# Kernel tuning notes

Hardware: AMD Instinct MI355X
Metric: run time of the kernel (lower is better)

Reference implementation:

```python
import jax, jax.numpy as jnp
import numpy as np

N = 200000   # total atoms in batched graph
E = 3200000  # total bonds (directed edges)
B = 512      # number of graphs / sequences
L = 1000     # miRNA sequence length


def _gcn(x, W, b, src, dst, dis):
    # PyG GCNConv: add self-loops, symmetric normalization D^-1/2 A D^-1/2
    h = x @ W                                   # [N, Fout]
    msg = (dis[src] * dis[dst])[:, None] * h[src]
    agg = jax.ops.segment_sum(msg, dst, num_segments=x.shape[0])
    return agg + (dis * dis)[:, None] * h + b   # self-loop term + bias


def _conv1d(x, k, b):
    # x: [B, C, L], k: [O, I, K]  (torch Conv1d, VALID padding)
    y = jax.lax.conv_general_dilated(x, k, (1,), 'VALID',
                                     dimension_numbers=('NCH', 'OIH', 'NCH'))
    return y + b[None, :, None]


def _mp3(x):
    # torch MaxPool1d(3): window 3, stride 3, floor
    return jax.lax.reduce_window(x, -jnp.inf, jax.lax.max, (1, 1, 3), (1, 1, 3), 'VALID')


def setup_inputs() -> dict:
    key = jax.random.key(0)
    ks = jax.random.split(key, 24)
    w = lambda k, s: (jax.random.normal(k, s, jnp.float32) * 0.1)
    p = {}
    p['x'] = jax.random.normal(ks[0], (N, 4), jnp.float32)
    p['edge_index'] = jax.random.randint(ks[1], (2, E), 0, N, jnp.int32)
    p['batch'] = (jnp.arange(N, dtype=jnp.int32) * B // N).astype(jnp.int32)  # every graph non-empty
    p['target'] = jax.random.normal(ks[2], (B, L, 5), jnp.float32)
    # GCN layers 4->4->8->16
    p['W1'] = w(ks[3], (4, 4));    p['b1'] = jnp.zeros(4, jnp.float32)
    p['W2'] = w(ks[4], (4, 8));    p['b2'] = jnp.zeros(8, jnp.float32)
    p['W3'] = w(ks[5], (8, 16));   p['b3'] = jnp.zeros(16, jnp.float32)
    p['Wg1'] = w(ks[6], (16, 1024)); p['bg1'] = jnp.zeros(1024, jnp.float32)
    p['Wg2'] = w(ks[7], (1024, 128)); p['bg2'] = jnp.zeros(128, jnp.float32)
    # CNN stack on sequences, kernels [O, I, 8]
    p['K1'] = w(ks[8], (32, 5, 8));   p['cb1'] = jnp.zeros(32, jnp.float32)
    p['K2'] = w(ks[9], (64, 32, 8));  p['cb2'] = jnp.zeros(64, jnp.float32)
    p['K3'] = w(ks[10], (128, 64, 8)); p['cb3'] = jnp.zeros(128, jnp.float32)
    p['Wxt'] = w(ks[11], (128, 128)); p['bxt'] = jnp.zeros(128, jnp.float32)
    # fusion head
    p['Wf1'] = w(ks[12], (256, 1024)); p['bf1'] = jnp.zeros(1024, jnp.float32)
    p['Wf2'] = w(ks[13], (1024, 512)); p['bf2'] = jnp.zeros(512, jnp.float32)
    p['Wo'] = w(ks[14], (512, 2));     p['bo'] = jnp.zeros(2, jnp.float32)
    return p


def reference(x, edge_index, batch, target, W1, b1, W2, b2, W3, b3,
              Wg1, bg1, Wg2, bg2, K1, cb1, K2, cb2, K3, cb3,
              Wxt, bxt, Wf1, bf1, Wf2, bf2, Wo, bo):
    src, dst = edge_index[0], edge_index[1]
    deg = jax.ops.segment_sum(jnp.ones(src.shape[0], x.dtype), dst,
                              num_segments=x.shape[0]) + 1.0  # +1 self-loop
    dis = jax.lax.rsqrt(deg)
    # Graph branch (dropout is identity in eval)
    h = jax.nn.relu(_gcn(x, W1, b1, src, dst, dis))
    h = jax.nn.relu(_gcn(h, W2, b2, src, dst, dis))
    h = jax.nn.relu(_gcn(h, W3, b3, src, dst, dis))
    g = jax.ops.segment_max(h, batch, num_segments=B)  # global_max_pool
    g = jax.nn.relu(g @ Wg1 + bg1)
    g = g @ Wg2 + bg2
    # Sequence branch
    t = jnp.transpose(target, (0, 2, 1))  # [B, 5, L]
    c = _mp3(jax.nn.relu(_conv1d(t, K1, cb1)))
    c = _mp3(jax.nn.relu(_conv1d(c, K2, cb2)))
    c = _mp3(jax.nn.relu(_conv1d(c, K3, cb3)))
    c = jnp.mean(c, axis=2)               # [B, 128]
    c = jax.nn.relu(c @ Wxt + bxt)
    # Fusion head
    xc = jnp.concatenate([g, c], axis=1)  # [B, 256]
    xc = jax.nn.relu(xc @ Wf1 + bf1)
    xc = jax.nn.relu(xc @ Wf2 + bf2)
    return xc @ Wo + bo                    # [B, 2]
```

## Files before the change

kernel.cpp:

```cpp
#include <hip/hip_runtime.h>
#include <hip/hip_fp16.h>
#include <cstddef>

#define NA 200000
#define NE 3200000
#define NB 512
#define NBKT 256
#define BKTN 782
#define BKTCAP 16384
#define NEPB 3200
#define NGB 3125

typedef _Float16 hv2 __attribute__((ext_vector_type(2)));
typedef _Float16 half8 __attribute__((ext_vector_type(8)));
typedef float floatx4 __attribute__((ext_vector_type(4)));
union UH2 { unsigned u; __half2 h; hv2 v; };
__device__ __forceinline__ float4 h4f(unsigned a, unsigned b) {
    UH2 x, y; x.u = a; y.u = b;
    float2 fa = __half22float2(x.h), fb = __half22float2(y.h);
    return make_float4(fa.x, fa.y, fb.x, fb.y);
}
__device__ __forceinline__ unsigned f2h(float a, float b) {
    UH2 r; r.h = __float22half2_rn(make_float2(a, b));
    return r.u;
}

__global__ void k_init(unsigned* g, int* gcursor,
                       float* gvec, const float* __restrict__ bg2,
                       float* xf2, const float* __restrict__ bf2,
                       float* xf1, const float* __restrict__ bf1,
                       const float* __restrict__ K2, const float* __restrict__ K3,
                       __half* __restrict__ Wt2, __half* __restrict__ Wt3) {
    int i = blockIdx.x * blockDim.x + threadIdx.x;
    if (i < NB * 16) g[i] = 0u;
    if (i < NBKT) gcursor[i] = i * BKTCAP;
    if (i < NB * 128) gvec[i] = bg2[i & 127];
    if (i < NB * 512) xf2[i] = bf2[i & 511];
    if (i < NB * 1024) xf1[i] = bf1[i & 1023];
    if (i < 64 * 32 * 8) {
        int o = i >> 8, rem = i & 255, c = rem >> 3, kk = rem & 7;
        Wt2[(o << 8) + (kk << 5) + c] = __float2half(K2[i]);
    }
    if (i < 128 * 64 * 8) {
        int o = i >> 9, rem = i & 511, c = rem >> 3, kk = rem & 7;
        Wt3[(o << 9) + (kk << 6) + c] = __float2half(K3[i]);
    }
}

template<int CIN, int COUT, int OBLK, int LIN, int PITCH, int POUT, int NTT>
__device__ __forceinline__ void dev_conv1(int b, int oy,
        const float* __restrict__ in, const float* __restrict__ Kw,
        const float* __restrict__ bias, __half* __restrict__ out,
        float* s_in) {
    constexpr int SPO = 256 / OBLK;
    constexpr int PT = (NTT < 4) ? NTT : 4;
    constexpr int NPASS = (NTT + PT - 1) / PT;
    for (int idx = threadIdx.x; idx < CIN * PITCH; idx += 256) s_in[idx] = 0.f;
    __syncthreads();
    for (int idx = threadIdx.x; idx < LIN * CIN; idx += 256) {
        int p = idx / CIN, c = idx - p * CIN;
        s_in[c * PITCH + p] = in[(size_t)b * (LIN * CIN) + idx];
    }
    __syncthreads();
    int ol = threadIdx.x / SPO;
    int s  = threadIdx.x - ol * SPO;
    int o  = oy * OBLK + ol;
    float bo = bias[o];
    const float* wrow = Kw + (size_t)o * CIN * 8;
    for (int pass = 0; pass < NPASS; pass++) {
        float acc[PT][12];
#pragma unroll
        for (int tt = 0; tt < PT; tt++)
#pragma unroll
            for (int j = 0; j < 12; j++) acc[tt][j] = 0.f;
        bool vld[PT]; int tgs[PT];
#pragma unroll
        for (int tt = 0; tt < PT; tt++) {
            int ta = pass * PT + tt;
            int tg = s + SPO * ta;
            tgs[tt] = tg;
            vld[tt] = (ta < NTT) && (4 * tg < POUT);
        }
        for (int i = 0; i < CIN; i++) {
            float wa[8];
            const float4* wp = (const float4*)(wrow + (size_t)i * 8);
            *(float4*)&wa[0] = wp[0];
            *(float4*)&wa[4] = wp[1];
#pragma unroll
            for (int tt = 0; tt < PT; tt++) {
                if (vld[tt]) {
                    const float4* xr = (const float4*)&s_in[i * PITCH + 12 * tgs[tt]];
                    float xa[20];
#pragma unroll
                    for (int q = 0; q < 5; q++) *(float4*)&xa[4 * q] = xr[q];
#pragma unroll
                    for (int j = 0; j < 12; j++) {
                        float sm = acc[tt][j];
#pragma unroll
                        for (int k = 0; k < 8; k++) sm = fmaf(xa[j + k], wa[k], sm);
                        acc[tt][j] = sm;
                    }
                }
            }
        }
#pragma unroll
        for (int tt = 0; tt < PT; tt++) {
            if (vld[tt]) {
#pragma unroll
                for (int p = 0; p < 4; p++) {
                    int P = 4 * tgs[tt] + p;
                    if (P < POUT) {
                        float m = fmaxf(fmaxf(acc[tt][3 * p], acc[tt][3 * p + 1]), acc[tt][3 * p + 2]);
                        out[((size_t)b * COUT + o) * POUT + P] = __float2half(fmaxf(m + bo, 0.f));
                    }
                }
            }
        }
    }
}

__device__ __forceinline__ void dev_conv2_mfma(int b,
        const __half* __restrict__ pool1, const __half* __restrict__ Wt2,
        const float* __restrict__ cb2, __half* __restrict__ pool2t,
        char* smem) {
    __half* sT   = (__half*)smem;
    __half* outS = (__half*)smem;
    const __half* inp = pool1 + (size_t)b * (32 * 331);
    for (int idx = threadIdx.x; idx < 32 * 331; idx += 256) {
        int c = idx / 331;
        int p = idx - c * 331;
        sT[p * 40 + c] = inp[idx];
    }
    __syncthreads();
    int lane = threadIdx.x & 63, wv = threadIdx.x >> 6;
    int l15 = lane & 15, lg = lane >> 4;
    int mtBeg = wv * 5;
    int nmt = (wv == 3) ? 6 : 5;
    const floatx4 FZ = {0.f, 0.f, 0.f, 0.f};
    floatx4 acc[6][4];
#pragma unroll
    for (int mi = 0; mi < 6; mi++)
#pragma unroll
        for (int nt = 0; nt < 4; nt++) acc[mi][nt] = FZ;
    const half8* WB = (const half8*)Wt2;
    for (int s = 0; s < 8; s++) {
        half8 bfr[4];
#pragma unroll
        for (int nt = 0; nt < 4; nt++)
            bfr[nt] = WB[(nt * 16 + l15) * 32 + s * 4 + lg];
        half8 afr[6];
#pragma unroll
        for (int mi = 0; mi < 6; mi++) {
            if (mi < nmt) {
                int row = (mtBeg + mi) * 16 + l15 + s;
                afr[mi] = *(const half8*)(sT + row * 40 + lg * 8);
            }
        }
#pragma unroll
        for (int mi = 0; mi < 6; mi++) {
            if (mi < nmt) {
#pragma unroll
                for (int nt = 0; nt < 4; nt++)
                    acc[mi][nt] = __builtin_amdgcn_mfma_f32_16x16x32_f16(
                        afr[mi], bfr[nt], acc[mi][nt], 0, 0, 0);
            }
        }
    }
    __syncthreads();
    float bo[4];
#pragma unroll
    for (int nt = 0; nt < 4; nt++) bo[nt] = cb2[nt * 16 + l15];
#pragma unroll
    for (int mi = 0; mi < 6; mi++) {
        if (mi < nmt) {
#pragma unroll
            for (int nt = 0; nt < 4; nt++) {
                int o = nt * 16 + l15;
#pragma unroll
                for (int r = 0; r < 4; r++) {
                    int p = (mtBeg + mi) * 16 + lg * 4 + r;
                    float v = fmaxf(acc[mi][nt][r] + bo[nt], 0.f);
                    outS[p * 68 + o] = __float2half(v);
                }
            }
        }
    }
    __syncthreads();
    __half* op = pool2t + (size_t)b * (108 * 64);
    for (int idx = threadIdx.x; idx < 108 * 64; idx += 256) {
        int P = idx >> 6, o = idx & 63;
        float v0 = __half2float(outS[(3 * P) * 68 + o]);
        float v1 = __half2float(outS[(3 * P + 1) * 68 + o]);
        float v2 = __half2float(outS[(3 * P + 2) * 68 + o]);
        op[idx] = __float2half(fmaxf(fmaxf(v0, v1), v2));
    }
}

__device__ __forceinline__ void dev_conv3_mfma(int b, int nh,
        const __half* __restrict__ pool2t, const __half* __restrict__ Wt3,
        const float* __restrict__ cb3, float* __restrict__ pool3,
        char* smem) {
    __half* sT  = (__half*)smem;
    float* outS = (float*)smem;
    const uint4* inp = (const uint4*)(pool2t + (size_t)b * (108 * 64));
    for (int t = threadIdx.x; t < 108 * 8; t += 256) {
        int r = t >> 3, s8 = t & 7;
        *(uint4*)(sT + r * 72 + s8 * 8) = inp[t];
    }
    __syncthreads();
    int lane = threadIdx.x & 63, wv = threadIdx.x >> 6;
    int l15 = lane & 15, lg = lane >> 4;
    int mtBeg = wv * 2;
    int nmt = (wv == 3) ? 1 : 2;
    const floatx4 FZ = {0.f, 0.f, 0.f, 0.f};
    floatx4 acc[2][4];
#pragma unroll
    for (int mi = 0; mi < 2; mi++)
#pragma unroll
        for (int nt = 0; nt < 4; nt++) acc[mi][nt] = FZ;
    const half8* WB = (const half8*)Wt3;
    for (int s = 0; s < 16; s++) {
        half8 afr[2];
#pragma unroll
        for (int mi = 0; mi < 2; mi++) {
            if (mi < nmt) {
                int row = (mtBeg + mi) * 16 + l15 + (s >> 1);
                afr[mi] = *(const half8*)(sT + row * 72 + (s & 1) * 32 + lg * 8);
            }
        }
#pragma unroll
        for (int nt = 0; nt < 4; nt++) {
            half8 bfr = WB[((nh * 4 + nt) * 16 + l15) * 64 + s * 4 + lg];
            acc[0][nt] = __builtin_amdgcn_mfma_f32_16x16x32_f16(
                afr[0], bfr, acc[0][nt], 0, 0, 0);
            if (nmt > 1)
                acc[1][nt] = __builtin_amdgcn_mfma_f32_16x16x32_f16(
                    afr[1], bfr, acc[1][nt], 0, 0, 0);
        }
    }
    __syncthreads();
    float bo[4];
#pragma unroll
    for (int nt = 0; nt < 4; nt++) bo[nt] = cb3[(nh * 4 + nt) * 16 + l15];
    float* op = pool3 + (size_t)b * (33 * 128);
    for (int pp = 0; pp < 3; pp++) {
        int t0 = 3 * pp;
#pragma unroll
        for (int mi = 0; mi < 2; mi++) {
            int tile = mtBeg + mi;
            if (mi < nmt && tile >= t0 && tile < t0 + 3) {
#pragma unroll
                for (int nt = 0; nt < 4; nt++) {
                    int ol = nt * 16 + l15;
#pragma unroll
                    for (int r = 0; r < 4; r++) {
                        int p = tile * 16 + lg * 4 + r;
                        if (p < 100)
                            outS[(p - 48 * pp) * 68 + ol] =
                                fmaxf(acc[mi][nt][r] + bo[nt], 0.f);
                    }
                }
            }
        }
        __syncthreads();
        int nP = (pp == 2) ? 1 : 16;
        for (int idx = threadIdx.x; idx < nP * 64; idx += 256) {
            int Pl = idx >> 6, ol = idx & 63;
            int P = 16 * pp + Pl;
            int p = 3 * P - 48 * pp;
            float v0 = outS[p * 68 + ol];
            float v1 = outS[(p + 1) * 68 + ol];
            float v2 = outS[(p + 2) * 68 + ol];
            op[P * 128 + (nh << 6) + ol] = fmaxf(fmaxf(v0, v1), v2);
        }
        __syncthreads();
    }
}

__global__ __launch_bounds__(256) void k_A(
        const int* __restrict__ src, const int* __restrict__ dst,
        int* __restrict__ gcursor, unsigned* __restrict__ stage,
        const float* __restrict__ tgt, const float* __restrict__ K1,
        const float* __restrict__ cb1, __half* __restrict__ pool1) {
    __shared__ __align__(16) char smem[20160];
    int bx = blockIdx.x;
    if (bx < 1024) {
        dev_conv1<5, 32, 16, 1000, 1008, 331, 6>(bx >> 1, bx & 1, tgt, K1, cb1,
                                                 pool1, (float*)smem);
        return;
    }
    int* hcnt  = (int*)smem;
    int* hbase = hcnt + 256;
    int* lbase = hbase + 256;
    unsigned* sbuf = (unsigned*)(lbase + 256);
    unsigned char* sbkt = (unsigned char*)(sbuf + NEPB);
    int t = threadIdx.x;
    int e0 = (bx - 1024) * NEPB;
    hcnt[t] = 0;
    __syncthreads();
    const int4* d4 = (const int4*)(dst + e0);
    for (int i = t; i < NEPB / 4; i += 256) {
        int4 d = d4[i];
        atomicAdd(&hcnt[d.x / BKTN], 1);
        atomicAdd(&hcnt[d.y / BKTN], 1);
        atomicAdd(&hcnt[d.z / BKTN], 1);
        atomicAdd(&hcnt[d.w / BKTN], 1);
    }
    __syncthreads();
    int myc = hcnt[t];
    hbase[t] = atomicAdd(&gcursor[t], myc);
    __syncthreads();
#pragma unroll
    for (int off = 1; off < 256; off <<= 1) {
        int u = (t >= off) ? hcnt[t - off] : 0;
        __syncthreads();
        hcnt[t] += u;
        __syncthreads();
    }
    lbase[t] = hcnt[t] - myc;
    hcnt[t] = 0;
    __syncthreads();
    const int4* s4 = (const int4*)(src + e0);
    for (int i = t; i < NEPB / 4; i += 256) {
        int4 d = d4[i];
        int4 s = s4[i];
        int ds[4] = {d.x, d.y, d.z, d.w};
        int ss[4] = {s.x, s.y, s.z, s.w};
#pragma unroll
        for (int j = 0; j < 4; j++) {
            int bkt = ds[j] / BKTN;
            int dloc = ds[j] - bkt * BKTN;
            int k = atomicAdd(&hcnt[bkt], 1);
            int pos = lbase[bkt] + k;
            sbuf[pos] = ((unsigned)dloc << 18) | (unsigned)ss[j];
            sbkt[pos] = (unsigned char)bkt;
        }
    }
    __syncthreads();
    for (int i = t; i < NEPB; i += 256) {
        unsigned v = sbuf[i];
        int bkt = sbkt[i];
        stage[hbase[bkt] + (i - lbase[bkt])] = v;
    }
}

__global__ __launch_bounds__(256) void k_Bp(
        const unsigned* __restrict__ stage, const int* __restrict__ gcursor,
        int* __restrict__ rowptr, int* __restrict__ cnt, int* __restrict__ csr,
        const float* __restrict__ x, float4* __restrict__ dt1) {
    __shared__ int lcnt[BKTN];
    __shared__ int lpos[BKTN];
    __shared__ int partial[256];
    __shared__ int sbase;
    int t = threadIdx.x;
    int bkt = blockIdx.x;
    int tot = gcursor[t] - t * BKTCAP;
    partial[t] = tot;
    __syncthreads();
#pragma unroll
    for (int off = 1; off < 256; off <<= 1) {
        int u = (t >= off) ? partial[t - off] : 0;
        __syncthreads();
        partial[t] += u;
        __syncthreads();
    }
    if (t == 0) sbase = (bkt == 0) ? 0 : partial[bkt - 1];
    __syncthreads();
    int base = sbase;
    int n0 = bkt * BKTN;
    int ncnt = (NA - n0 < BKTN) ? (NA - n0) : BKTN;
    int eBeg = bkt * BKTCAP;
    int eCnt = gcursor[bkt] - eBeg;
    for (int i = t; i < BKTN; i += 256) lcnt[i] = 0;
    __syncthreads();
    for (int i = t; i < eCnt; i += 256)
        atomicAdd(&lcnt[stage[eBeg + i] >> 18], 1);
    __syncthreads();
    int mysum = 0;
#pragma unroll
    for (int j = 0; j < 4; j++) {
        int node = 4 * t + j;
        if (node < ncnt) mysum += lcnt[node];
    }
    partial[t] = mysum;
    __syncthreads();
#pragma unroll
    for (int off = 1; off < 256; off <<= 1) {
        int u = (t >= off) ? partial[t - off] : 0;
        __syncthreads();
        partial[t] += u;
        __syncthreads();
    }
    int running = partial[t] - mysum;
#pragma unroll
    for (int j = 0; j < 4; j++) {
        int node = 4 * t + j;
        if (node < ncnt) {
            lpos[node] = running;
            rowptr[n0 + node] = base + running;
            cnt[n0 + node] = lcnt[node];
            running += lcnt[node];
        }
    }
    __syncthreads();
    for (int i = t; i < eCnt; i += 256) {
        unsigned v = stage[eBeg + i];
        int dloc = v >> 18;
        int s = v & 0x3FFFF;
        int k = atomicAdd(&lpos[dloc], 1);
        csr[base + k] = s;
    }
    for (int i = t; i < ncnt; i += 256) {
        int n = n0 + i;
        float4 p = ((const float4*)x)[n];
        float dv = rsqrtf((float)lcnt[i] + 1.0f);
        dt1[n] = make_float4(dv * p.x, dv * p.y, dv * p.z, dv * p.w);
    }
}

__global__ __launch_bounds__(256) void k_B(
        const __half* __restrict__ pool1, const __half* __restrict__ Wt2,
        const float* __restrict__ cb2, __half* __restrict__ pool2t,
        const float4* __restrict__ dt1, const int* __restrict__ rowptr,
        const int* __restrict__ cnt, const int* __restrict__ csr,
        const float* __restrict__ W1, const float* __restrict__ b1,
        float* __restrict__ dt2f) {
    __shared__ __align__(16) char smem[45696];
    int bx = blockIdx.x;
    if (bx < 512) {
        dev_conv2_mfma(bx, pool1, Wt2, cb2, pool2t, smem);
        return;
    }
    __shared__ float sW[16];
    if (threadIdx.x < 16) sW[threadIdx.x] = W1[threadIdx.x];
    __syncthreads();
    int n   = (bx - 512) * 64 + (threadIdx.x >> 2);
    int sub = threadIdx.x & 3;
    int cn = cnt[n];
    float dv = rsqrtf((float)cn + 1.0f);
    const int* row = csr + rowptr[n];
    float4 selfv = dt1[n];
    float4 acc = make_float4(0.f, 0.f, 0.f, 0.f);
    if (sub == 0) acc = selfv;
    int e = sub;
    for (; e + 12 < cn; e += 16) {
        float4 v0 = dt1[row[e]];
        float4 v1 = dt1[row[e + 4]];
        float4 v2 = dt1[row[e + 8]];
        float4 v3 = dt1[row[e + 12]];
        acc.x += (v0.x + v1.x) + (v2.x + v3.x);
        acc.y += (v0.y + v1.y) + (v2.y + v3.y);
        acc.z += (v0.z + v1.z) + (v2.z + v3.z);
        acc.w += (v0.w + v1.w) + (v2.w + v3.w);
    }
    for (; e < cn; e += 4) {
        float4 v = dt1[row[e]];
        acc.x += v.x; acc.y += v.y; acc.z += v.z; acc.w += v.w;
    }
    acc.x += __shfl_xor(acc.x, 1); acc.y += __shfl_xor(acc.y, 1);
    acc.z += __shfl_xor(acc.z, 1); acc.w += __shfl_xor(acc.w, 1);
    acc.x += __shfl_xor(acc.x, 2); acc.y += __shfl_xor(acc.y, 2);
    acc.z += __shfl_xor(acc.z, 2); acc.w += __shfl_xor(acc.w, 2);
    float a[4] = {acc.x, acc.y, acc.z, acc.w};
    float s = 0.f;
#pragma unroll
    for (int k = 0; k < 4; k++) s = fmaf(a[k], sW[k * 4 + sub], s);
    float o = dv * fmaxf(fmaf(dv, s, b1[sub]), 0.f);
    dt2f[(size_t)n * 4 + sub] = o;
}

__global__ __launch_bounds__(256, 8) void k_C(
        const __half* __restrict__ pool2t, const __half* __restrict__ Wt3,
        const float* __restrict__ cb3, float* __restrict__ pool3,
        const float4* __restrict__ dt2, const int* __restrict__ rowptr,
        const int* __restrict__ cnt, const int* __restrict__ csr,
        const float* __restrict__ W2, const float* __restrict__ b2,
        unsigned* __restrict__ dt3u) {
    __shared__ __align__(16) char smem[17280];
    int bx = blockIdx.x;
    if (bx < 1024) {
        dev_conv3_mfma(bx & 511, bx >> 9, pool2t, Wt3, cb3, pool3, smem);
        return;
    }
    __shared__ float sW[32];
    if (threadIdx.x < 32) sW[threadIdx.x] = W2[threadIdx.x];
    __syncthreads();
    int n   = (bx - 1024) * 64 + (threadIdx.x >> 2);
    int sub = threadIdx.x & 3;
    int cn = cnt[n];
    float dv = rsqrtf((float)cn + 1.0f);
    const int* row = csr + rowptr[n];
    float4 selfv = dt2[n];
    float4 acc = make_float4(0.f, 0.f, 0.f, 0.f);
    if (sub == 0) acc = selfv;
    int e = sub;
    for (; e + 12 < cn; e += 16) {
        float4 v0 = dt2[row[e]];
        float4 v1 = dt2[row[e + 4]];
        float4 v2 = dt2[row[e + 8]];
        float4 v3 = dt2[row[e + 12]];
        acc.x += (v0.x + v1.x) + (v2.x + v3.x);
        acc.y += (v0.y + v1.y) + (v2.y + v3.y);
        acc.z += (v0.z + v1.z) + (v2.z + v3.z);
        acc.w += (v0.w + v1.w) + (v2.w + v3.w);
    }
    for (; e < cn; e += 4) {
        float4 v = dt2[row[e]];
        acc.x += v.x; acc.y += v.y; acc.z += v.z; acc.w += v.w;
    }
    acc.x += __shfl_xor(acc.x, 1); acc.y += __shfl_xor(acc.y, 1);
    acc.z += __shfl_xor(acc.z, 1); acc.w += __shfl_xor(acc.w, 1);
    acc.x += __shfl_xor(acc.x, 2); acc.y += __shfl_xor(acc.y, 2);
    acc.z += __shfl_xor(acc.z, 2); acc.w += __shfl_xor(acc.w, 2);
    float a[4] = {acc.x, acc.y, acc.z, acc.w};
    int f0 = 2 * sub;
    float s0 = 0.f, s1 = 0.f;
#pragma unroll
    for (int k = 0; k < 4; k++) {
        s0 = fmaf(a[k], sW[k * 8 + f0], s0);
        s1 = fmaf(a[k], sW[k * 8 + f0 + 1], s1);
    }
    float o0 = dv * fmaxf(fmaf(dv, s0, b2[f0]), 0.f);
    float o1 = dv * fmaxf(fmaf(dv, s1, b2[f0 + 1]), 0.f);
    dt3u[(size_t)n * 4 + sub] = f2h(o0, o1);
}

__global__ __launch_bounds__(256) void k_D(
        const uint4* __restrict__ dt3, const int* __restrict__ rowptr,
        const int* __restrict__ cnt, const int* __restrict__ csr,
        const float* __restrict__ W3, const float* __restrict__ b3,
        const int* __restrict__ batch, unsigned* __restrict__ g,
        const float* __restrict__ pool3, const float* __restrict__ Wxt,
        const float* __restrict__ bxt, float* __restrict__ cx) {
    int bx = blockIdx.x;
    if (bx >= NGB) {
        __shared__ float sa[8 * 128];
        int b0 = (bx - NGB) * 8;
        for (int t = threadIdx.x; t < 8 * 128; t += 256) {
            int gg = t >> 7, k = t & 127;
            const float* r = pool3 + (size_t)(b0 + gg) * (33 * 128) + k;
            float s = 0.f;
#pragma unroll
            for (int p = 0; p < 33; p++) s += r[p * 128];
            sa[t] = s * (1.f / 33.f);
        }
        __syncthreads();
        int j = threadIdx.x;
        if (j >= 128) return;
        float bj = bxt[j];
        float acc[8];
#pragma unroll
        for (int gg = 0; gg < 8; gg++) acc[gg] = bj;
#pragma unroll 4
        for (int k = 0; k < 128; k++) {
            float w = Wxt[(size_t)k * 128 + j];
#pragma unroll
            for (int gg = 0; gg < 8; gg++) acc[gg] = fmaf(sa[gg * 128 + k], w, acc[gg]);
        }
#pragma unroll
        for (int gg = 0; gg < 8; gg++)
            cx[(size_t)(b0 + gg) * 128 + j] = fmaxf(acc[gg], 0.f);
        return;
    }
    __shared__ float sW[128];
    __shared__ unsigned sg[32];
    __shared__ int sbmin;
    if (threadIdx.x < 128) sW[threadIdx.x] = W3[threadIdx.x];
    if (threadIdx.x < 32) sg[threadIdx.x] = 0u;
    if (threadIdx.x == 0) sbmin = batch[bx * 64];
    __syncthreads();
    int n   = bx * 64 + (threadIdx.x >> 2);
    int sub = threadIdx.x & 3;
    int cn = cnt[n];
    float dv = rsqrtf((float)cn + 1.0f);
    const int* row = csr + rowptr[n];
    uint4 sv = dt3[n];
    float4 slo = h4f(sv.x, sv.y), shi = h4f(sv.z, sv.w);
    float a0 = 0.f, a1 = 0.f, a2 = 0.f, a3 = 0.f;
    float a4 = 0.f, a5 = 0.f, a6 = 0.f, a7 = 0.f;
    if (sub == 0) {
        a0 = slo.x; a1 = slo.y; a2 = slo.z; a3 = slo.w;
        a4 = shi.x; a5 = shi.y; a6 = shi.z; a7 = shi.w;
    }
    int e = sub;
    for (; e + 12 < cn; e += 16) {
        uint4 p0 = dt3[row[e]], p1 = dt3[row[e + 4]];
        uint4 p2 = dt3[row[e + 8]], p3 = dt3[row[e + 12]];
        float4 l0 = h4f(p0.x, p0.y), h0 = h4f(p0.z, p0.w);
        float4 l1 = h4f(p1.x, p1.y), h1 = h4f(p1.z, p1.w);
        float4 l2 = h4f(p2.x, p2.y), h2 = h4f(p2.z, p2.w);
        float4 l3 = h4f(p3.x, p3.y), h3v = h4f(p3.z, p3.w);
        a0 += (l0.x + l1.x) + (l2.x + l3.x);
        a1 += (l0.y + l1.y) + (l2.y + l3.y);
        a2 += (l0.z + l1.z) + (l2.z + l3.z);
        a3 += (l0.w + l1.w) + (l2.w + l3.w);
        a4 += (h0.x + h1.x) + (h2.x + h3v.x);
        a5 += (h0.y + h1.y) + (h2.y + h3v.y);
        a6 += (h0.z + h1.z) + (h2.z + h3v.z);
        a7 += (h0.w + h1.w) + (h2.w + h3v.w);
    }
    for (; e < cn; e += 4) {
        uint4 p = dt3[row[e]];
        float4 l = h4f(p.x, p.y), h = h4f(p.z, p.w);
        a0 += l.x; a1 += l.y; a2 += l.z; a3 += l.w;
        a4 += h.x; a5 += h.y; a6 += h.z; a7 += h.w;
    }
    a0 += __shfl_xor(a0, 1); a1 += __shfl_xor(a1, 1);
    a2 += __shfl_xor(a2, 1); a3 += __shfl_xor(a3, 1);
    a4 += __shfl_xor(a4, 1); a5 += __shfl_xor(a5, 1);
    a6 += __shfl_xor(a6, 1); a7 += __shfl_xor(a7, 1);
    a0 += __shfl_xor(a0, 2); a1 += __shfl_xor(a1, 2);
    a2 += __shfl_xor(a2, 2); a3 += __shfl_xor(a3, 2);
    a4 += __shfl_xor(a4, 2); a5 += __shfl_xor(a5, 2);
    a6 += __shfl_xor(a6, 2); a7 += __shfl_xor(a7, 2);
    float af[8] = {a0, a1, a2, a3, a4, a5, a6, a7};
    int rb = batch[n] - sbmin;
    if (rb > 1) rb = 1;
#pragma unroll
    for (int j = 0; j < 4; j++) {
        int f = sub * 4 + j;
        float s = 0.f;
#pragma unroll
        for (int k = 0; k < 8; k++) s = fmaf(af[k], sW[k * 16 + f], s);
        float r = fmaxf(fmaf(dv, s, b3[f]), 0.f);
        atomicMax(&sg[rb * 16 + f], __float_as_uint(r));
    }
    __syncthreads();
    if (threadIdx.x < 32) {
        unsigned v = sg[threadIdx.x];
        int rb2 = threadIdx.x >> 4, f = threadIdx.x & 15;
        int bbn = sbmin + rb2;
        if (v != 0u && bbn < NB) atomicMax(&g[bbn * 16 + f], v);
    }
}

__global__ __launch_bounds__(256) void k_head_g(
        const float* __restrict__ g, const float* __restrict__ Wg1,
        const float* __restrict__ bg1, float* __restrict__ gp1) {
    __shared__ float sa[8 * 16];
    int bx = blockIdx.x;
    int b0 = (bx >> 2) * 8;
    if (threadIdx.x < 128)
        sa[threadIdx.x] = g[b0 * 16 + threadIdx.x];
    __syncthreads();
    int j = (bx & 3) * 256 + threadIdx.x;
    float bj = bg1[j];
    float acc[8];
#pragma unroll
    for (int gg = 0; gg < 8; gg++) acc[gg] = bj;
#pragma unroll
    for (int k = 0; k < 16; k++) {
        float w = Wg1[(size_t)k * 1024 + j];
#pragma unroll
        for (int gg = 0; gg < 8; gg++) acc[gg] = fmaf(sa[gg * 16 + k], w, acc[gg]);
    }
#pragma unroll
    for (int gg = 0; gg < 8; gg++)
        gp1[(size_t)(b0 + gg) * 1024 + j] = fmaxf(acc[gg], 0.f);
}

__global__ __launch_bounds__(256) void k_gvec_ks(
        const float* __restrict__ gp1, const float* __restrict__ Wg2,
        float* __restrict__ gvec) {
    __shared__ float sa[8 * 128];
    int k0 = blockIdx.x * 128;
    int b0 = blockIdx.y * 8;
    for (int t = threadIdx.x; t < 8 * 128; t += 256) {
        int gg = t >> 7, k = t & 127;
        sa[t] = gp1[(size_t)(b0 + gg) * 1024 + k0 + k];
    }
    __syncthreads();
    int j  = threadIdx.x & 127;
    int kh = (threadIdx.x >> 7) * 64;
    const float* Wp = Wg2 + (size_t)(k0 + kh) * 128 + j;
    float acc[8];
#pragma unroll
    for (int gg = 0; gg < 8; gg++) acc[gg] = 0.f;
    for (int k = 0; k < 64; k += 16) {
        float w[16];
#pragma unroll
        for (int u = 0; u < 16; u++) w[u] = Wp[(size_t)(k + u) * 128];
#pragma unroll
        for (int u = 0; u < 16; u++) {
#pragma unroll
            for (int gg = 0; gg < 8; gg++)
                acc[gg] = fmaf(sa[gg * 128 + kh + k + u], w[u], acc[gg]);
        }
    }
#pragma unroll
    for (int gg = 0; gg < 8; gg++)
        atomicAdd(&gvec[(size_t)(b0 + gg) * 128 + j], acc[gg]);
}

__global__ __launch_bounds__(256) void k_cat2(
        const float* __restrict__ gvec, const float* __restrict__ cx,
        const float* __restrict__ Wf1, float* __restrict__ xf1) {
    __shared__ float sa[8 * 128];
    int jx = blockIdx.x & 3;
    int kh = blockIdx.x >> 2;
    int b0 = blockIdx.y * 8;
    const float* A = kh ? cx : gvec;
    for (int t = threadIdx.x; t < 8 * 128; t += 256) {
        int gg = t >> 7, k = t & 127;
        sa[t] = A[(size_t)(b0 + gg) * 128 + k];
    }
    __syncthreads();
    int j = jx * 256 + threadIdx.x;
    const float* Wp = Wf1 + (size_t)(kh * 128) * 1024 + j;
    float acc[8];
#pragma unroll
    for (int gg = 0; gg < 8; gg++) acc[gg] = 0.f;
    for (int k = 0; k < 128; k += 16) {
        float w[16];
#pragma unroll
        for (int u = 0; u < 16; u++) w[u] = Wp[(size_t)(k + u) * 1024];
#pragma unroll
        for (int u = 0; u < 16; u++) {
#pragma unroll
            for (int gg = 0; gg < 8; gg++)
                acc[gg] = fmaf(sa[gg * 128 + k + u], w[u], acc[gg]);
        }
    }
#pragma unroll
    for (int gg = 0; gg < 8; gg++)
        atomicAdd(&xf1[(size_t)(b0 + gg) * 1024 + j], acc[gg]);
}

__global__ __launch_bounds__(256) void k_xf2_ks(
        const float* __restrict__ xf1, const float* __restrict__ Wf2,
        float* __restrict__ xf2) {
    __shared__ float sa[8 * 256];
    int jb = blockIdx.x & 1;
    int k0 = (blockIdx.x >> 1) * 256;
    int b0 = blockIdx.y * 8;
    for (int t = threadIdx.x; t < 8 * 256; t += 256) {
        int gg = t >> 8, k = t & 255;
        sa[t] = fmaxf(xf1[(size_t)(b0 + gg) * 1024 + k0 + k], 0.f);
    }
    __syncthreads();
    int j = jb * 256 + threadIdx.x;
    const float* Wp = Wf2 + (size_t)k0 * 512 + j;
    float acc[8];
#pragma unroll
    for (int gg = 0; gg < 8; gg++) acc[gg] = 0.f;
    for (int k = 0; k < 256; k += 16) {
        float w[16];
#pragma unroll
        for (int u = 0; u < 16; u++) w[u] = Wp[(size_t)(k + u) * 512];
#pragma unroll
        for (int u = 0; u < 16; u++) {
#pragma unroll
            for (int gg = 0; gg < 8; gg++)
                acc[gg] = fmaf(sa[gg * 256 + k + u], w[u], acc[gg]);
        }
    }
#pragma unroll
    for (int gg = 0; gg < 8; gg++)
        atomicAdd(&xf2[(size_t)(b0 + gg) * 512 + j], acc[gg]);
}

__global__ __launch_bounds__(256) void k_dense_out(
        const float* __restrict__ A, const float* __restrict__ W,
        const float* __restrict__ bias, float* __restrict__ out) {
    int idx = blockIdx.x * 256 + threadIdx.x;
    if (idx >= NB * 2) return;
    int b = idx >> 1, j = idx & 1;
    float s = bias[j];
    const float4* A4 = (const float4*)(A + (size_t)b * 512);
    for (int k4 = 0; k4 < 128; k4 += 8) {
        float4 av[8];
#pragma unroll
        for (int u = 0; u < 8; u++) av[u] = A4[k4 + u];
#pragma unroll
        for (int u = 0; u < 8; u++) {
            int kb = (k4 + u) * 4;
            s = fmaf(fmaxf(av[u].x, 0.f), W[(kb + 0) * 2 + j], s);
            s = fmaf(fmaxf(av[u].y, 0.f), W[(kb + 1) * 2 + j], s);
            s = fmaf(fmaxf(av[u].z, 0.f), W[(kb + 2) * 2 + j], s);
            s = fmaf(fmaxf(av[u].w, 0.f), W[(kb + 3) * 2 + j], s);
        }
    }
    out[idx] = s;
}

extern "C" void kernel_launch(void* const* d_in, const int* in_sizes, int n_in,
                              void* d_out, int out_size, void* d_ws, size_t ws_size,
                              hipStream_t stream) {
    (void)in_sizes; (void)n_in; (void)out_size; (void)ws_size;
    const float* x   = (const float*)d_in[0];
    const int*  ei   = (const int*)d_in[1];
    const int*  batch= (const int*)d_in[2];
    const float* tgt = (const float*)d_in[3];
    const float* W1  = (const float*)d_in[4];  const float* b1  = (const float*)d_in[5];
    const float* W2  = (const float*)d_in[6];  const float* b2  = (const float*)d_in[7];
    const float* W3  = (const float*)d_in[8];  const float* b3  = (const float*)d_in[9];
    const float* Wg1 = (const float*)d_in[10]; const float* bg1 = (const float*)d_in[11];
    const float* Wg2 = (const float*)d_in[12]; const float* bg2 = (const float*)d_in[13];
    const float* K1  = (const float*)d_in[14]; const float* cb1 = (const float*)d_in[15];
    const float* K2  = (const float*)d_in[16]; const float* cb2 = (const float*)d_in[17];
    const float* K3  = (const float*)d_in[18]; const float* cb3 = (const float*)d_in[19];
    const float* Wxt = (const float*)d_in[20]; const float* bxt = (const float*)d_in[21];
    const float* Wf1 = (const float*)d_in[22]; const float* bf1 = (const float*)d_in[23];
    const float* Wf2 = (const float*)d_in[24]; const float* bf2 = (const float*)d_in[25];
    const float* Wo  = (const float*)d_in[26]; const float* bo  = (const float*)d_in[27];
    const int* srcp = ei;
    const int* dstp = ei + NE;

    float* ws = (float*)d_ws;
    float4* dt1 = (float4*)ws; ws += (size_t)NA * 4;
    float4* dt2 = (float4*)ws; ws += (size_t)NA * 4;
    uint4*  dt3 = (uint4*)ws;  ws += (size_t)NA * 4;
    float* g     = ws; ws += NB * 16;
    float* gp1   = ws; ws += NB * 1024;
    float* gvec  = ws; ws += NB * 128;
    float* cx    = ws; ws += NB * 128;
    float* xf1   = ws; ws += NB * 1024;
    float* xf2   = ws; ws += NB * 512;
    __half* pool1 = (__half*)ws; ws += (size_t)NB * 32 * 331;
    __half* pool2t = (__half*)ws; ws += (size_t)NB * 64 * 108;
    float* pool3 = ws; ws += (size_t)NB * 128 * 33;
    __half* Wt2 = (__half*)ws; ws += 64 * 256 / 2;
    __half* Wt3 = (__half*)ws; ws += 128 * 512 / 2;
    int*   cnt    = (int*)ws; ws += NA;
    int*   rowptr = (int*)ws; ws += NA;
    int*   csr    = (int*)ws; ws += NE;
    int*   gcursor= (int*)ws; ws += NBKT;
    unsigned* stage = (unsigned*)ws; ws += (size_t)NBKT * BKTCAP;

    dim3 blk(256);

    k_init<<<2048, blk, 0, stream>>>((unsigned*)g, gcursor, gvec, bg2, xf2, bf2,
                                     xf1, bf1, K2, K3, Wt2, Wt3);
    k_A<<<2024, blk, 0, stream>>>(srcp, dstp, gcursor, stage, tgt, K1, cb1, pool1);
    k_Bp<<<256, blk, 0, stream>>>(stage, gcursor, rowptr, cnt, csr, x, dt1);
    k_B<<<512 + NGB, blk, 0, stream>>>(pool1, Wt2, cb2, pool2t,
                                       dt1, rowptr, cnt, csr, W1, b1, (float*)dt2);
    k_C<<<1024 + NGB, blk, 0, stream>>>(pool2t, Wt3, cb3, pool3,
                                        dt2, rowptr, cnt, csr, W2, b2, (unsigned*)dt3);
    k_D<<<NGB + 64, blk, 0, stream>>>(dt3, rowptr, cnt, csr, W3, b3,
                                      batch, (unsigned*)g, pool3, Wxt, bxt, cx);

    k_head_g<<<256, blk, 0, stream>>>(g, Wg1, bg1, gp1);
    k_gvec_ks<<<dim3(8, 64), blk, 0, stream>>>(gp1, Wg2, gvec);
    k_cat2<<<dim3(8, 64), blk, 0, stream>>>(gvec, cx, Wf1, xf1);
    k_xf2_ks<<<dim3(8, 64), blk, 0, stream>>>(xf1, Wf2, xf2);
    k_dense_out<<<4, blk, 0, stream>>>(xf2, Wo, bo, (float*)d_out);
}
```

Baseline: 393.9 us.

## Move first conv1d layer onto MFMA f16 matrix cores with im2col-style fragments

Replaces the scalar FP32 direct convolution for the first Conv1d (5->32 channels, kernel 8) with an MFMA 16x16x32 f16 implementation. Input channels are padded to 8 and the weights are pre-packed into an fp16 buffer in the init kernel. Each block now covers a third of a sequence instead of half the output channels, and the conv blocks are placed after the edge-bucketing blocks in the fused launch. The change trades FP32 precision for fp16 inputs and adds extra shared-memory staging for the pooling step.

After: 402.0 us. +2.1%, slower.

```diff
diff --git a/kernel.cpp b/kernel.cpp
--- a/kernel.cpp
+++ b/kernel.cpp
@@ -29,14 +29,21 @@
                        float* gvec, const float* __restrict__ bg2,
                        float* xf2, const float* __restrict__ bf2,
                        float* xf1, const float* __restrict__ bf1,
-                       const float* __restrict__ K2, const float* __restrict__ K3,
-                       __half* __restrict__ Wt2, __half* __restrict__ Wt3) {
+                       const float* __restrict__ K1, const float* __restrict__ K2,
+                       const float* __restrict__ K3,
+                       __half* __restrict__ Wt1, __half* __restrict__ Wt2,
+                       __half* __restrict__ Wt3) {
     int i = blockIdx.x * blockDim.x + threadIdx.x;
     if (i < NB * 16) g[i] = 0u;
     if (i < NBKT) gcursor[i] = i * BKTCAP;
     if (i < NB * 128) gvec[i] = bg2[i & 127];
     if (i < NB * 512) xf2[i] = bf2[i & 511];
     if (i < NB * 1024) xf1[i] = bf1[i & 1023];
+    if (i < 32 * 64) {
+        int o = i >> 6, k = i & 63, kk = k >> 3, c = k & 7;
+        Wt1[i] = (c < 5) ? __float2half(K1[(o * 5 + c) * 8 + kk])
+                         : __float2half(0.f);
+    }
     if (i < 64 * 32 * 8) {
         int o = i >> 8, rem = i & 255, c = rem >> 3, kk = rem & 7;
         Wt2[(o << 8) + (kk << 5) + c] = __float2half(K2[i]);
@@ -47,74 +54,82 @@
     }
 }
 
-template<int CIN, int COUT, int OBLK, int LIN, int PITCH, int POUT, int NTT>
-__device__ __forceinline__ void dev_conv1(int b, int oy,
-        const float* __restrict__ in, const float* __restrict__ Kw,
-        const float* __restrict__ bias, __half* __restrict__ out,
-        float* s_in) {
-    constexpr int SPO = 256 / OBLK;
-    constexpr int PT = (NTT < 4) ? NTT : 4;
-    constexpr int NPASS = (NTT + PT - 1) / PT;
-    for (int idx = threadIdx.x; idx < CIN * PITCH; idx += 256) s_in[idx] = 0.f;
-    __syncthreads();
-    for (int idx = threadIdx.x; idx < LIN * CIN; idx += 256) {
-        int p = idx / CIN, c = idx - p * CIN;
-        s_in[c * PITCH + p] = in[(size_t)b * (LIN * CIN) + idx];
-    }
-    __syncthreads();
-    int ol = threadIdx.x / SPO;
-    int s  = threadIdx.x - ol * SPO;
-    int o  = oy * OBLK + ol;
-    float bo = bias[o];
-    const float* wrow = Kw + (size_t)o * CIN * 8;
-    for (int pass = 0; pass < NPASS; pass++) {
-        float acc[PT][12];
-#pragma unroll
-        for (int tt = 0; tt < PT; tt++)
-#pragma unroll
-            for (int j = 0; j < 12; j++) acc[tt][j] = 0.f;
-        bool vld[PT]; int tgs[PT];
-#pragma unroll
-        for (int tt = 0; tt < PT; tt++) {
-            int ta = pass * PT + tt;
-            int tg = s + SPO * ta;
-            tgs[tt] = tg;
-            vld[tt] = (ta < NTT) && (4 * tg < POUT);
-        }
-        for (int i = 0; i < CIN; i++) {
-            float wa[8];
-            const float4* wp = (const float4*)(wrow + (size_t)i * 8);
-            *(float4*)&wa[0] = wp[0];
-            *(float4*)&wa[4] = wp[1];
-#pragma unroll
-            for (int tt = 0; tt < PT; tt++) {
-                if (vld[tt]) {
-                    const float4* xr = (const float4*)&s_in[i * PITCH + 12 * tgs[tt]];
-                    float xa[20];
-#pragma unroll
-                    for (int q = 0; q < 5; q++) *(float4*)&xa[4 * q] = xr[q];
-#pragma unroll
-                    for (int j = 0; j < 12; j++) {
-                        float sm = acc[tt][j];
-#pragma unroll
-                        for (int k = 0; k < 8; k++) sm = fmaf(xa[j + k], wa[k], sm);
-                        acc[tt][j] = sm;
-                    }
+__device__ __forceinline__ void dev_conv1_mfma(int b, int pp,
+        const float* __restrict__ tgt, const __half* __restrict__ Wt1,
+        const float* __restrict__ cb1, __half* __restrict__ pool1,
+        char* smem) {
+    __half* sIn  = (__half*)smem;
+    __half* outS = (__half*)smem;
+    int base = pp * 336;
+    for (int idx = threadIdx.x; idx < 344 * 8; idx += 256) {
+        int pl = idx >> 3, c = idx & 7;
+        int gp = base + pl;
+        float v = (c < 5 && gp < 1000) ? tgt[(size_t)b * 5000 + gp * 5 + c] : 0.f;
+        sIn[idx] = __float2half(v);
+    }
+    __syncthreads();
+    int lane = threadIdx.x & 63, wv = threadIdx.x >> 6;
+    int l15 = lane & 15, lg = lane >> 4;
+    int mtBeg = wv * 5;
+    int nmt = (wv == 3) ? 6 : 5;
+    const floatx4 FZ = {0.f, 0.f, 0.f, 0.f};
+    floatx4 acc[6][2];
+#pragma unroll
+    for (int mi = 0; mi < 6; mi++)
+#pragma unroll
+        for (int nt = 0; nt < 2; nt++) acc[mi][nt] = FZ;
+    const half8* WB = (const half8*)Wt1;
+#pragma unroll
+    for (int s = 0; s < 2; s++) {
+        half8 bfr[2];
+#pragma unroll
+        for (int nt = 0; nt < 2; nt++)
+            bfr[nt] = WB[(nt * 16 + l15) * 8 + s * 4 + lg];
+        half8 afr[6];
+#pragma unroll
+        for (int mi = 0; mi < 6; mi++) {
+            if (mi < nmt) {
+                int row = (mtBeg + mi) * 16 + l15 + s * 4 + lg;
+                afr[mi] = *(const half8*)(sIn + row * 8);
+            }
+        }
+#pragma unroll
+        for (int mi = 0; mi < 6; mi++) {
+            if (mi < nmt) {
+#pragma unroll
+                for (int nt = 0; nt < 2; nt++)
+                    acc[mi][nt] = __builtin_amdgcn_mfma_f32_16x16x32_f16(
+                        afr[mi], bfr[nt], acc[mi][nt], 0, 0, 0);
+            }
+        }
+    }
+    __syncthreads();
+#pragma unroll
+    for (int mi = 0; mi < 6; mi++) {
+        if (mi < nmt) {
+#pragma unroll
+            for (int nt = 0; nt < 2; nt++) {
+                int o = nt * 16 + l15;
+#pragma unroll
+                for (int r = 0; r < 4; r++) {
+                    int p = (mtBeg + mi) * 16 + lg * 4 + r;
+                    outS[p * 36 + o] = __float2half(acc[mi][nt][r]);
                 }
             }
         }
-#pragma unroll
-        for (int tt = 0; tt < PT; tt++) {
-            if (vld[tt]) {
-#pragma unroll
-                for (int p = 0; p < 4; p++) {
-                    int P = 4 * tgs[tt] + p;
-                    if (P < POUT) {
-                        float m = fmaxf(fmaxf(acc[tt][3 * p], acc[tt][3 * p + 1]), acc[tt][3 * p + 2]);
-                        out[((size_t)b * COUT + o) * POUT + P] = __float2half(fmaxf(m + bo, 0.f));
-                    }
-                }
-            }
+    }
+    __syncthreads();
+    __half* op = pool1 + (size_t)b * (32 * 331);
+    for (int idx = threadIdx.x; idx < 112 * 32; idx += 256) {
+        int P = idx >> 5, o = idx & 31;
+        int Pg = pp * 112 + P;
+        if (Pg < 331) {
+            int p = 3 * P;
+            float v0 = __half2float(outS[p * 36 + o]);
+            float v1 = __half2float(outS[(p + 1) * 36 + o]);
+            float v2 = __half2float(outS[(p + 2) * 36 + o]);
+            float m = fmaxf(fmaxf(v0, v1), v2);
+            op[o * 331 + Pg] = __float2half(fmaxf(m + cb1[o], 0.f));
         }
     }
 }
@@ -280,13 +295,13 @@
 __global__ __launch_bounds__(256) void k_A(
         const int* __restrict__ src, const int* __restrict__ dst,
         int* __restrict__ gcursor, unsigned* __restrict__ stage,
-        const float* __restrict__ tgt, const float* __restrict__ K1,
+        const float* __restrict__ tgt, const __half* __restrict__ Wt1,
         const float* __restrict__ cb1, __half* __restrict__ pool1) {
-    __shared__ __align__(16) char smem[20160];
+    __shared__ __align__(16) char smem[24192];
     int bx = blockIdx.x;
-    if (bx < 1024) {
-        dev_conv1<5, 32, 16, 1000, 1008, 331, 6>(bx >> 1, bx & 1, tgt, K1, cb1,
-                                                 pool1, (float*)smem);
+    if (bx >= 1000) {
+        int ci = bx - 1000;
+        dev_conv1_mfma(ci & 511, ci >> 9, tgt, Wt1, cb1, pool1, smem);
         return;
     }
     int* hcnt  = (int*)smem;
@@ -295,7 +310,7 @@
     unsigned* sbuf = (unsigned*)(lbase + 256);
     unsigned char* sbkt = (unsigned char*)(sbuf + NEPB);
     int t = threadIdx.x;
-    int e0 = (bx - 1024) * NEPB;
+    int e0 = bx * NEPB;
     hcnt[t] = 0;
     __syncthreads();
     const int4* d4 = (const int4*)(dst + e0);
@@ -819,6 +834,7 @@
     __half* pool1 = (__half*)ws; ws += (size_t)NB * 32 * 331;
     __half* pool2t = (__half*)ws; ws += (size_t)NB * 64 * 108;
     float* pool3 = ws; ws += (size_t)NB * 128 * 33;
+    __half* Wt1 = (__half*)ws; ws += 32 * 64 / 2;
     __half* Wt2 = (__half*)ws; ws += 64 * 256 / 2;
     __half* Wt3 = (__half*)ws; ws += 128 * 512 / 2;
     int*   cnt    = (int*)ws; ws += NA;
@@ -830,8 +846,8 @@
     dim3 blk(256);
 
     k_init<<<2048, blk, 0, stream>>>((unsigned*)g, gcursor, gvec, bg2, xf2, bf2,
-                                     xf1, bf1, K2, K3, Wt2, Wt3);
-    k_A<<<2024, blk, 0, stream>>>(srcp, dstp, gcursor, stage, tgt, K1, cb1, pool1);
+                                     xf1, bf1, K1, K2, K3, Wt1, Wt2, Wt3);
+    k_A<<<2536, blk, 0, stream>>>(srcp, dstp, gcursor, stage, tgt, Wt1, cb1, pool1);
     k_Bp<<<256, blk, 0, stream>>>(stage, gcursor, rowptr, cnt, csr, x, dt1);
     k_B<<<512 + NGB, blk, 0, stream>>>(pool1, Wt2, cb2, pool2t,
                                        dt1, rowptr, cnt, csr, W1, b1, (float*)dt2);
```
